# Kernel tuning notes

Hardware: AMD Instinct MI355X
Metric: run time of the kernel (lower is better)

The kernel has to match this reference:

```python
import jax, jax.numpy as jnp
import numpy as np

NUM_STEPS = 151


def setup_inputs() -> dict:
    key = jax.random.key(0)
    k1, k2 = jax.random.split(key)
    feats = jax.random.normal(k1, (1024, 128), dtype=jnp.float32)
    # dists must lie in [-1, 1] -> L2-normalize embeddings (cosine similarity)
    feats = feats / jnp.linalg.norm(feats, axis=1, keepdims=True)
    classes = jax.random.randint(k2, (1024,), 0, 100, dtype=jnp.int32)
    return {"features": feats, "classes": classes}


def reference(features, classes):
    n = features.shape[0]
    step = 2.0 / (NUM_STEPS - 1)
    # bin centers t_j = -1 + j*step, j = 0..NUM_STEPS-1 (torch.range(-1, 1, step))
    t = (-1.0 + jnp.arange(NUM_STEPS, dtype=jnp.float32) * step)[:, None]  # [T,1]

    dists = features @ features.T                      # [N,N]
    iu = jnp.triu_indices(n, k=1)                      # strict upper triangle
    s = dists[iu]                                      # [P] pairwise similarities
    eq = (classes[:, None] == classes[None, :])[iu]    # [P] same-class mask

    pos_size = jnp.sum(eq).astype(jnp.float32)
    neg_size = jnp.sum(~eq).astype(jnp.float32)

    # snap each similarity to the bin edge below it (detached, like .data in torch)
    delta = jnp.floor((jax.lax.stop_gradient(s) + 1.0) / step) * step - 1.0  # [P]

    indsa = delta[None, :] == (t - step)   # s falls in [t-step, t): rising edge
    indsb = delta[None, :] == t            # s falls in [t, t+step): falling edge
    wa = (s[None, :] - t + step) / step
    wb = (-s[None, :] + t + step) / step
    w = jnp.where(indsa, wa, jnp.where(indsb, wb, 0.0))  # [T,P] triangular weights

    hist_pos = jnp.sum(jnp.where(eq[None, :], w, 0.0), axis=1) / pos_size  # [T]
    hist_neg = jnp.sum(jnp.where(eq[None, :], 0.0, w), axis=1) / neg_size  # [T]

    # tril(ones,-1) zeroing + sum over dim 0 == inclusive cumulative sum
    hist_pos_cdf = jnp.cumsum(hist_pos)
    loss = jnp.sum(hist_neg * hist_pos_cdf)
    return loss
```

## Files before the change

### kernel.cpp

```cpp
#include <hip/hip_runtime.h>

#define T_STEPS 151
#define NN 1024
#define DD 128
#define TILE 32
#define NTILE (NN / TILE)
#define NBLOCKS (NTILE * (NTILE + 1) / 2)
#define LDSTRIDE 132
#define NCOPY 8
#define WSROW 304
#define NPAIRS 523776.0f


__global__ __launch_bounds__(256) void hist_kernel(
    const float* __restrict__ F, const int* __restrict__ cls, float* __restrict__ ws)
{
    __shared__ float As[TILE][LDSTRIDE];
    __shared__ float Bs[TILE][LDSTRIDE];
    __shared__ float hpos[T_STEPS];
    __shared__ float hneg[T_STEPS];
    __shared__ int   clsA[TILE];
    __shared__ int   clsB[TILE];
    __shared__ float pcount;

    const int t = threadIdx.x;

    int rem = blockIdx.x;
    int bi = 0;
    while (rem >= (NTILE - bi)) { rem -= (NTILE - bi); ++bi; }
    const int bj = bi + rem;

    for (int k = t; k < T_STEPS; k += 256) { hpos[k] = 0.f; hneg[k] = 0.f; }
    if (t == 0) pcount = 0.f;
    if (t < TILE)            clsA[t]        = cls[bi * TILE + t];
    else if (t < 2 * TILE)   clsB[t - TILE] = cls[bj * TILE + (t - TILE)];

    const float* Abase = F + (size_t)bi * TILE * DD;
    const float* Bbase = F + (size_t)bj * TILE * DD;
    for (int idx = t; idx < TILE * DD / 4; idx += 256) {
        int r = idx >> 5;
        int c = (idx & 31) << 2;
        *(float4*)&As[r][c] = *(const float4*)(Abase + r * DD + c);
        *(float4*)&Bs[r][c] = *(const float4*)(Bbase + r * DD + c);
    }
    __syncthreads();

    const int r2 = t >> 4;
    const int c2 = t & 15;

    float acc[2][2][4];
    #pragma unroll
    for (int a = 0; a < 2; ++a)
        #pragma unroll
        for (int b = 0; b < 2; ++b)
            #pragma unroll
            for (int q = 0; q < 4; ++q) acc[a][b][q] = 0.f;

    #pragma unroll 4
    for (int k = 0; k < DD; k += 4) {
        float4 a0 = *(const float4*)&As[r2][k];
        float4 a1 = *(const float4*)&As[r2 + 16][k];
        float4 b0 = *(const float4*)&Bs[c2][k];
        float4 b1 = *(const float4*)&Bs[c2 + 16][k];
        acc[0][0][0] += a0.x * b0.x; acc[0][0][1] += a0.y * b0.y;
        acc[0][0][2] += a0.z * b0.z; acc[0][0][3] += a0.w * b0.w;
        acc[0][1][0] += a0.x * b1.x; acc[0][1][1] += a0.y * b1.y;
        acc[0][1][2] += a0.z * b1.z; acc[0][1][3] += a0.w * b1.w;
        acc[1][0][0] += a1.x * b0.x; acc[1][0][1] += a1.y * b0.y;
        acc[1][0][2] += a1.z * b0.z; acc[1][0][3] += a1.w * b0.w;
        acc[1][1][0] += a1.x * b1.x; acc[1][1][1] += a1.y * b1.y;
        acc[1][1][2] += a1.z * b1.z; acc[1][1][3] += a1.w * b1.w;
    }

    const float STEP = 2.0f / 150.0f;
    float myp = 0.f;
    {
        #pragma clang fp contract(off)
        #pragma unroll
        for (int ii = 0; ii < 2; ++ii) {
            #pragma unroll
            for (int jj = 0; jj < 2; ++jj) {
                int gi = bi * TILE + r2 + 16 * ii;
                int gj = bj * TILE + c2 + 16 * jj;
                if (gi < gj) {
                    float* a = acc[ii][jj];
                    float s = (a[0] + a[1]) + (a[2] + a[3]);
                    bool eqf = (clsA[r2 + 16 * ii] == clsB[c2 + 16 * jj]);
                    float kf    = floorf((s + 1.0f) / STEP);
                    float delta = kf * STEP - 1.0f;
                    int   kk    = (int)kf;
                    if (kk >= 0 && kk < T_STEPS) {
                        float tk = -1.0f + (float)kk * STEP;
                        if (delta == tk) {
                            float wb = (-s + tk + STEP) / STEP;
                            unsafeAtomicAdd(eqf ? &hpos[kk] : &hneg[kk], wb);
                        }
                    }
                    int k1 = kk + 1;
                    if (k1 >= 0 && k1 < T_STEPS) {
                        float tk1 = -1.0f + (float)k1 * STEP;
                        if (delta == (tk1 - STEP)) {
                            float wa = (s - tk1 + STEP) / STEP;
                            unsafeAtomicAdd(eqf ? &hpos[k1] : &hneg[k1], wa);
                        }
                    }
                    if (eqf) myp += 1.f;
                }
            }
        }
    }
    #pragma unroll
    for (int off = 32; off > 0; off >>= 1) myp += __shfl_down(myp, off, 64);
    if ((t & 63) == 0) unsafeAtomicAdd(&pcount, myp);
    __syncthreads();

    float* copy = ws + (size_t)(blockIdx.x & (NCOPY - 1)) * WSROW;
    for (int k = t; k < T_STEPS; k += 256) {
        float hp = hpos[k], hn = hneg[k];
        if (hp != 0.f) unsafeAtomicAdd(&copy[k], hp);
        if (hn != 0.f) unsafeAtomicAdd(&copy[T_STEPS + k], hn);
    }
    if (t == 0) unsafeAtomicAdd(&copy[2 * T_STEPS], pcount);
}

__global__ __launch_bounds__(256) void final_kernel(
    const float* __restrict__ ws, float* __restrict__ out)
{
    __shared__ float hsum[2 * T_STEPS];
    __shared__ float possh;
    const int t = threadIdx.x;

    const unsigned int pu = 0xAAAAAAAAu;
    const float P8 = 8.0f * __uint_as_float(pu);

    for (int k = t; k <= 2 * T_STEPS; k += 256) {
        float v = 0.f;
        #pragma unroll
        for (int c = 0; c < NCOPY; ++c) v += ws[c * WSROW + k];
        v -= P8;
        if (k < 2 * T_STEPS) hsum[k] = v;
        else                 possh   = v;
    }
    __syncthreads();
    {
        #pragma clang fp contract(off)
        float pos = possh;
        float neg = NPAIRS - pos;
        for (int k = t; k < 2 * T_STEPS; k += 256)
            hsum[k] = hsum[k] / (k < T_STEPS ? pos : neg);
    }
    __syncthreads();
    if (t == 0) {
        #pragma clang fp contract(off)
        float cdf = 0.f, loss = 0.f;
        for (int j = 0; j < T_STEPS; ++j) {
            cdf  += hsum[j];
            loss += hsum[T_STEPS + j] * cdf;
        }
        out[0] = loss;
    }
}

extern "C" void kernel_launch(void* const* d_in, const int* in_sizes, int n_in,
                              void* d_out, int out_size, void* d_ws, size_t ws_size,
                              hipStream_t stream)
{
    const float* F   = (const float*)d_in[0];
    const int*   cls = (const int*)d_in[1];
    float*       ws  = (float*)d_ws;
    float*       out = (float*)d_out;

    hist_kernel<<<NBLOCKS, 256, 0, stream>>>(F, cls, ws);
    final_kernel<<<1, 256, 0, stream>>>(ws, out);
}
```

Before: 69.18 us.

## Shrink hist blocks to one wavefront with a 4x4 per-thread register tile

The histogram kernel now launches one 64-thread wavefront per 32x32 tile instead of 256 threads. Each thread computes a 4x4 block of dot products, which raises register reuse of the LDS-loaded float4 vectors and removes the shared pcount atomic because a wave shuffle reduction now covers the whole block. The trade-off is fewer threads to hide latency of the global loads and LDS traffic, more registers per thread, and more serial binning work per thread.

```diff
diff --git a/kernel.cpp b/kernel.cpp
--- a/kernel.cpp
+++ b/kernel.cpp
@@ -12,7 +12,7 @@
 #define NPAIRS 523776.0f
 
 
-__global__ __launch_bounds__(256) void hist_kernel(
+__global__ __launch_bounds__(64) void hist_kernel(
     const float* __restrict__ F, const int* __restrict__ cls, float* __restrict__ ws)
 {
     __shared__ float As[TILE][LDSTRIDE];
@@ -21,7 +21,6 @@
     __shared__ float hneg[T_STEPS];
     __shared__ int   clsA[TILE];
     __shared__ int   clsB[TILE];
-    __shared__ float pcount;
 
     const int t = threadIdx.x;
 
@@ -30,14 +29,13 @@
     while (rem >= (NTILE - bi)) { rem -= (NTILE - bi); ++bi; }
     const int bj = bi + rem;
 
-    for (int k = t; k < T_STEPS; k += 256) { hpos[k] = 0.f; hneg[k] = 0.f; }
-    if (t == 0) pcount = 0.f;
-    if (t < TILE)            clsA[t]        = cls[bi * TILE + t];
-    else if (t < 2 * TILE)   clsB[t - TILE] = cls[bj * TILE + (t - TILE)];
+    for (int k = t; k < T_STEPS; k += 64) { hpos[k] = 0.f; hneg[k] = 0.f; }
+    if (t < TILE) clsA[t]        = cls[bi * TILE + t];
+    else          clsB[t - TILE] = cls[bj * TILE + (t - TILE)];
 
     const float* Abase = F + (size_t)bi * TILE * DD;
     const float* Bbase = F + (size_t)bj * TILE * DD;
-    for (int idx = t; idx < TILE * DD / 4; idx += 256) {
+    for (int idx = t; idx < TILE * DD / 4; idx += 64) {
         int r = idx >> 5;
         int c = (idx & 31) << 2;
         *(float4*)&As[r][c] = *(const float4*)(Abase + r * DD + c);
@@ -45,31 +43,34 @@
     }
     __syncthreads();
 
-    const int r2 = t >> 4;
-    const int c2 = t & 15;
+    const int tr = t >> 3;
+    const int tc = t & 7;
 
-    float acc[2][2][4];
+    float acc[4][4][4];
     #pragma unroll
-    for (int a = 0; a < 2; ++a)
+    for (int a = 0; a < 4; ++a)
         #pragma unroll
-        for (int b = 0; b < 2; ++b)
+        for (int b = 0; b < 4; ++b)
             #pragma unroll
             for (int q = 0; q < 4; ++q) acc[a][b][q] = 0.f;
 
-    #pragma unroll 4
+    #pragma unroll 2
     for (int k = 0; k < DD; k += 4) {
-        float4 a0 = *(const float4*)&As[r2][k];
-        float4 a1 = *(const float4*)&As[r2 + 16][k];
-        float4 b0 = *(const float4*)&Bs[c2][k];
-        float4 b1 = *(const float4*)&Bs[c2 + 16][k];
-        acc[0][0][0] += a0.x * b0.x; acc[0][0][1] += a0.y * b0.y;
-        acc[0][0][2] += a0.z * b0.z; acc[0][0][3] += a0.w * b0.w;
-        acc[0][1][0] += a0.x * b1.x; acc[0][1][1] += a0.y * b1.y;
-        acc[0][1][2] += a0.z * b1.z; acc[0][1][3] += a0.w * b1.w;
-        acc[1][0][0] += a1.x * b0.x; acc[1][0][1] += a1.y * b0.y;
-        acc[1][0][2] += a1.z * b0.z; acc[1][0][3] += a1.w * b0.w;
-        acc[1][1][0] += a1.x * b1.x; acc[1][1][1] += a1.y * b1.y;
-        acc[1][1][2] += a1.z * b1.z; acc[1][1][3] += a1.w * b1.w;
+        float4 av[4], bv[4];
+        #pragma unroll
+        for (int ii = 0; ii < 4; ++ii) av[ii] = *(const float4*)&As[tr + 8 * ii][k];
+        #pragma unroll
+        for (int jj = 0; jj < 4; ++jj) bv[jj] = *(const float4*)&Bs[tc + 8 * jj][k];
+        #pragma unroll
+        for (int ii = 0; ii < 4; ++ii) {
+            #pragma unroll
+            for (int jj = 0; jj < 4; ++jj) {
+                acc[ii][jj][0] += av[ii].x * bv[jj].x;
+                acc[ii][jj][1] += av[ii].y * bv[jj].y;
+                acc[ii][jj][2] += av[ii].z * bv[jj].z;
+                acc[ii][jj][3] += av[ii].w * bv[jj].w;
+            }
+        }
     }
 
     const float STEP = 2.0f / 150.0f;
@@ -77,15 +78,15 @@
     {
         #pragma clang fp contract(off)
         #pragma unroll
-        for (int ii = 0; ii < 2; ++ii) {
+        for (int ii = 0; ii < 4; ++ii) {
             #pragma unroll
-            for (int jj = 0; jj < 2; ++jj) {
-                int gi = bi * TILE + r2 + 16 * ii;
-                int gj = bj * TILE + c2 + 16 * jj;
+            for (int jj = 0; jj < 4; ++jj) {
+                int gi = bi * TILE + tr + 8 * ii;
+                int gj = bj * TILE + tc + 8 * jj;
                 if (gi < gj) {
                     float* a = acc[ii][jj];
                     float s = (a[0] + a[1]) + (a[2] + a[3]);
-                    bool eqf = (clsA[r2 + 16 * ii] == clsB[c2 + 16 * jj]);
+                    bool eqf = (clsA[tr + 8 * ii] == clsB[tc + 8 * jj]);
                     float kf    = floorf((s + 1.0f) / STEP);
                     float delta = kf * STEP - 1.0f;
                     int   kk    = (int)kf;
@@ -111,16 +112,15 @@
     }
     #pragma unroll
     for (int off = 32; off > 0; off >>= 1) myp += __shfl_down(myp, off, 64);
-    if ((t & 63) == 0) unsafeAtomicAdd(&pcount, myp);
     __syncthreads();
 
     float* copy = ws + (size_t)(blockIdx.x & (NCOPY - 1)) * WSROW;
-    for (int k = t; k < T_STEPS; k += 256) {
+    for (int k = t; k < T_STEPS; k += 64) {
         float hp = hpos[k], hn = hneg[k];
         if (hp != 0.f) unsafeAtomicAdd(&copy[k], hp);
         if (hn != 0.f) unsafeAtomicAdd(&copy[T_STEPS + k], hn);
     }
-    if (t == 0) unsafeAtomicAdd(&copy[2 * T_STEPS], pcount);
+    if (t == 0) unsafeAtomicAdd(&copy[2 * T_STEPS], myp);
 }
 
 __global__ __launch_bounds__(256) void final_kernel(
@@ -170,6 +170,6 @@
     float*       ws  = (float*)d_ws;
     float*       out = (float*)d_out;
 
-    hist_kernel<<<NBLOCKS, 256, 0, stream>>>(F, cls, ws);
+    hist_kernel<<<NBLOCKS, 64, 0, stream>>>(F, cls, ws);
     final_kernel<<<1, 256, 0, stream>>>(ws, out);
 }
```

After: 75.34 us. +8.9%, slower.

## Pack pairs of diagonal tiles into one block to balance work

Applied to the files above, without the earlier changes.

Replaces the triangular grid of 528 tile blocks with 496 off-diagonal blocks plus 16 blocks that each process two diagonal tiles. In those blocks each 128-thread half computes a full 32x32 self-product on its own tile, so no threads sit idle on masked lower-triangle entries. The binning logic moves into a shared helper. This cuts the launch to 512 blocks but adds a second code path and more registers per thread in the diagonal case.

```diff
diff --git a/kernel.cpp b/kernel.cpp
--- a/kernel.cpp
+++ b/kernel.cpp
@@ -5,12 +5,39 @@
 #define DD 128
 #define TILE 32
 #define NTILE (NN / TILE)
-#define NBLOCKS (NTILE * (NTILE + 1) / 2)
+#define NOFF 496
+#define NBLOCKS 512
 #define LDSTRIDE 132
 #define NCOPY 8
 #define WSROW 304
 #define NPAIRS 523776.0f
 
+
+__device__ __forceinline__ void bin_pair(
+    float s, bool eqf, float* __restrict__ hpos, float* __restrict__ hneg, float& myp)
+{
+    #pragma clang fp contract(off)
+    const float STEP = 2.0f / 150.0f;
+    float kf    = floorf((s + 1.0f) / STEP);
+    float delta = kf * STEP - 1.0f;
+    int   kk    = (int)kf;
+    if (kk >= 0 && kk < T_STEPS) {
+        float tk = -1.0f + (float)kk * STEP;
+        if (delta == tk) {
+            float wb = (-s + tk + STEP) / STEP;
+            unsafeAtomicAdd(eqf ? &hpos[kk] : &hneg[kk], wb);
+        }
+    }
+    int k1 = kk + 1;
+    if (k1 >= 0 && k1 < T_STEPS) {
+        float tk1 = -1.0f + (float)k1 * STEP;
+        if (delta == (tk1 - STEP)) {
+            float wa = (s - tk1 + STEP) / STEP;
+            unsafeAtomicAdd(eqf ? &hpos[k1] : &hneg[k1], wa);
+        }
+    }
+    if (eqf) myp += 1.f;
+}
 
 __global__ __launch_bounds__(256) void hist_kernel(
     const float* __restrict__ F, const int* __restrict__ cls, float* __restrict__ ws)
@@ -23,12 +50,20 @@
     __shared__ int   clsB[TILE];
     __shared__ float pcount;
 
-    const int t = threadIdx.x;
-
-    int rem = blockIdx.x;
-    int bi = 0;
-    while (rem >= (NTILE - bi)) { rem -= (NTILE - bi); ++bi; }
-    const int bj = bi + rem;
+    const int t   = threadIdx.x;
+    const int bid = blockIdx.x;
+
+    int bi, bj;
+    if (bid < NOFF) {
+        int rem = bid;
+        bi = 0;
+        while (rem >= (NTILE - 1 - bi)) { rem -= (NTILE - 1 - bi); ++bi; }
+        bj = bi + 1 + rem;
+    } else {
+        int m = bid - NOFF;
+        bi = 2 * m;
+        bj = 2 * m + 1;
+    }
 
     for (int k = t; k < T_STEPS; k += 256) { hpos[k] = 0.f; hneg[k] = 0.f; }
     if (t == 0) pcount = 0.f;
@@ -45,70 +80,104 @@
     }
     __syncthreads();
 
-    const int r2 = t >> 4;
-    const int c2 = t & 15;
-
-    float acc[2][2][4];
-    #pragma unroll
-    for (int a = 0; a < 2; ++a)
+    float myp = 0.f;
+
+    if (bid < NOFF) {
+        const int r2 = t >> 4;
+        const int c2 = t & 15;
+
+        float acc[2][2][4];
         #pragma unroll
-        for (int b = 0; b < 2; ++b)
-            #pragma unroll
-            for (int q = 0; q < 4; ++q) acc[a][b][q] = 0.f;
-
-    #pragma unroll 4
-    for (int k = 0; k < DD; k += 4) {
-        float4 a0 = *(const float4*)&As[r2][k];
-        float4 a1 = *(const float4*)&As[r2 + 16][k];
-        float4 b0 = *(const float4*)&Bs[c2][k];
-        float4 b1 = *(const float4*)&Bs[c2 + 16][k];
-        acc[0][0][0] += a0.x * b0.x; acc[0][0][1] += a0.y * b0.y;
-        acc[0][0][2] += a0.z * b0.z; acc[0][0][3] += a0.w * b0.w;
-        acc[0][1][0] += a0.x * b1.x; acc[0][1][1] += a0.y * b1.y;
-        acc[0][1][2] += a0.z * b1.z; acc[0][1][3] += a0.w * b1.w;
-        acc[1][0][0] += a1.x * b0.x; acc[1][0][1] += a1.y * b0.y;
-        acc[1][0][2] += a1.z * b0.z; acc[1][0][3] += a1.w * b0.w;
-        acc[1][1][0] += a1.x * b1.x; acc[1][1][1] += a1.y * b1.y;
-        acc[1][1][2] += a1.z * b1.z; acc[1][1][3] += a1.w * b1.w;
-    }
-
-    const float STEP = 2.0f / 150.0f;
-    float myp = 0.f;
-    {
-        #pragma clang fp contract(off)
-        #pragma unroll
-        for (int ii = 0; ii < 2; ++ii) {
-            #pragma unroll
-            for (int jj = 0; jj < 2; ++jj) {
-                int gi = bi * TILE + r2 + 16 * ii;
-                int gj = bj * TILE + c2 + 16 * jj;
-                if (gi < gj) {
+        for (int a = 0; a < 2; ++a)
+            #pragma unroll
+            for (int b = 0; b < 2; ++b)
+                #pragma unroll
+                for (int q = 0; q < 4; ++q) acc[a][b][q] = 0.f;
+
+        #pragma unroll 4
+        for (int k = 0; k < DD; k += 4) {
+            float4 a0 = *(const float4*)&As[r2][k];
+            float4 a1 = *(const float4*)&As[r2 + 16][k];
+            float4 b0 = *(const float4*)&Bs[c2][k];
+            float4 b1 = *(const float4*)&Bs[c2 + 16][k];
+            acc[0][0][0] += a0.x * b0.x; acc[0][0][1] += a0.y * b0.y;
+            acc[0][0][2] += a0.z * b0.z; acc[0][0][3] += a0.w * b0.w;
+            acc[0][1][0] += a0.x * b1.x; acc[0][1][1] += a0.y * b1.y;
+            acc[0][1][2] += a0.z * b1.z; acc[0][1][3] += a0.w * b1.w;
+            acc[1][0][0] += a1.x * b0.x; acc[1][0][1] += a1.y * b0.y;
+            acc[1][0][2] += a1.z * b0.z; acc[1][0][3] += a1.w * b0.w;
+            acc[1][1][0] += a1.x * b1.x; acc[1][1][1] += a1.y * b1.y;
+            acc[1][1][2] += a1.z * b1.z; acc[1][1][3] += a1.w * b1.w;
+        }
+
+        {
+            #pragma clang fp contract(off)
+            #pragma unroll
+            for (int ii = 0; ii < 2; ++ii) {
+                #pragma unroll
+                for (int jj = 0; jj < 2; ++jj) {
                     float* a = acc[ii][jj];
                     float s = (a[0] + a[1]) + (a[2] + a[3]);
                     bool eqf = (clsA[r2 + 16 * ii] == clsB[c2 + 16 * jj]);
-                    float kf    = floorf((s + 1.0f) / STEP);
-                    float delta = kf * STEP - 1.0f;
-                    int   kk    = (int)kf;
-                    if (kk >= 0 && kk < T_STEPS) {
-                        float tk = -1.0f + (float)kk * STEP;
-                        if (delta == tk) {
-                            float wb = (-s + tk + STEP) / STEP;
-                            unsafeAtomicAdd(eqf ? &hpos[kk] : &hneg[kk], wb);
-                        }
-                    }
-                    int k1 = kk + 1;
-                    if (k1 >= 0 && k1 < T_STEPS) {
-                        float tk1 = -1.0f + (float)k1 * STEP;
-                        if (delta == (tk1 - STEP)) {
-                            float wa = (s - tk1 + STEP) / STEP;
-                            unsafeAtomicAdd(eqf ? &hpos[k1] : &hneg[k1], wa);
-                        }
-                    }
-                    if (eqf) myp += 1.f;
+                    bin_pair(s, eqf, hpos, hneg, myp);
                 }
             }
         }
-    }
+    } else {
+        const int g  = t >> 7;
+        const int tt = t & 127;
+        const int r4 = tt >> 4;
+        const int c2 = tt & 15;
+
+        float (*P)[LDSTRIDE] = g ? Bs : As;
+        const int* clsP      = g ? clsB : clsA;
+
+        float acc[4][2][4];
+        #pragma unroll
+        for (int a = 0; a < 4; ++a)
+            #pragma unroll
+            for (int b = 0; b < 2; ++b)
+                #pragma unroll
+                for (int q = 0; q < 4; ++q) acc[a][b][q] = 0.f;
+
+        #pragma unroll 2
+        for (int k = 0; k < DD; k += 4) {
+            float4 av[4], bv[2];
+            #pragma unroll
+            for (int a = 0; a < 4; ++a) av[a] = *(const float4*)&P[r4 + 8 * a][k];
+            #pragma unroll
+            for (int b = 0; b < 2; ++b) bv[b] = *(const float4*)&P[c2 + 16 * b][k];
+            #pragma unroll
+            for (int a = 0; a < 4; ++a) {
+                #pragma unroll
+                for (int b = 0; b < 2; ++b) {
+                    acc[a][b][0] += av[a].x * bv[b].x;
+                    acc[a][b][1] += av[a].y * bv[b].y;
+                    acc[a][b][2] += av[a].z * bv[b].z;
+                    acc[a][b][3] += av[a].w * bv[b].w;
+                }
+            }
+        }
+
+        {
+            #pragma clang fp contract(off)
+            #pragma unroll
+            for (int a = 0; a < 4; ++a) {
+                #pragma unroll
+                for (int b = 0; b < 2; ++b) {
+                    int ri = r4 + 8 * a;
+                    int cj = c2 + 16 * b;
+                    if (ri < cj) {
+                        float* ac = acc[a][b];
+                        float s = (ac[0] + ac[1]) + (ac[2] + ac[3]);
+                        bool eqf = (clsP[ri] == clsP[cj]);
+                        bin_pair(s, eqf, hpos, hneg, myp);
+                    }
+                }
+            }
+        }
+    }
+
     #pragma unroll
     for (int off = 32; off > 0; off >>= 1) myp += __shfl_down(myp, off, 64);
     if ((t & 63) == 0) unsafeAtomicAdd(&pcount, myp);
```

Measured after the change: 69.16 us. No clear change (-0.0%).
